# Kernel optimization log

Hardware: AMD Instinct MI355X
Metric: run time of the kernel (lower is better)

## Reference

```python
import jax, jax.numpy as jnp
import numpy as np

GAMMA = 0.5
BATCH, DIM, UNITS = 16384, 512, 1024


def setup_inputs() -> dict:
    key = jax.random.key(0)
    k1, k2 = jax.random.split(key)
    inputs = jax.random.normal(k1, (BATCH, DIM), dtype=jnp.float32)
    mu = jax.random.normal(k2, (DIM, UNITS), dtype=jnp.float32)
    return {"inputs": inputs, "mu": mu}


def reference(inputs, mu):
    # Squared L2 distance from each input row to each center (column of mu):
    x_sq = jnp.sum(inputs * inputs, axis=1, keepdims=True)        # [B, 1]
    mu_sq = jnp.sum(mu * mu, axis=0, keepdims=True)               # [1, U]
    cross = inputs @ mu                                           # [B, U] GEMM
    l2 = x_sq - 2.0 * cross + mu_sq                                # [B, U]
    return jnp.exp(-GAMMA * l2)
```

## Files before the change

### kernel.cpp

```cpp
#include <hip/hip_runtime.h>
#include <hip/hip_bf16.h>

#define BATCH 16384
#define DIM   512
#define UNITS 1024

typedef float v16f __attribute__((ext_vector_type(16)));

__device__ __forceinline__ void async_copy16(const void* g, void* l) {
    __builtin_amdgcn_global_load_lds(
        (const __attribute__((address_space(1))) void*)g,
        (__attribute__((address_space(3))) void*)l,
        16 , 0 , 0 );
}

__global__ __launch_bounds__(256)
void prep_b_kernel(const float* __restrict__ mu, unsigned char* __restrict__ Bt,
                   float* __restrict__ musq) {
    __shared__ float lds[64][65];
    __shared__ float red[64][4];
    const int t  = threadIdx.x;
    const int n0 = blockIdx.x * 64;
    const int c  = t & 63, r4 = t >> 6;
    const int nl = t >> 2, kp = t & 3;
    float s = 0.f;
    for (int kc = 0; kc < DIM; kc += 64) {
        __syncthreads();
#pragma unroll
        for (int i = 0; i < 16; i++)
            lds[r4 + i * 4][c] = mu[(size_t)(kc + r4 + i * 4) * UNITS + n0 + c];
        __syncthreads();
        int wr[4];
#pragma unroll
        for (int q = 0; q < 4; q++) {
            float f0 = lds[kp * 16 + q * 4 + 0][nl];
            float f1 = lds[kp * 16 + q * 4 + 1][nl];
            float f2 = lds[kp * 16 + q * 4 + 2][nl];
            float f3 = lds[kp * 16 + q * 4 + 3][nl];
            s += f0 * f0 + f1 * f1 + f2 * f2 + f3 * f3;
            int v = __builtin_amdgcn_cvt_pk_fp8_f32(f0, f1, 0, false);
            wr[q]  = __builtin_amdgcn_cvt_pk_fp8_f32(f2, f3, v, true);
        }
        *(int4*)(Bt + (size_t)(n0 + nl) * DIM + kc + kp * 16) =
            make_int4(wr[0], wr[1], wr[2], wr[3]);
    }
    red[nl][kp] = s;
    __syncthreads();
    if (t < 64) musq[n0 + t] = red[t][0] + red[t][1] + red[t][2] + red[t][3];
}

__global__ __launch_bounds__(512, 2)
void rbf_gemm_kernel(const float* __restrict__ A,
                     const unsigned char* __restrict__ Bt,
                     const float* __restrict__ musq,
                     float* __restrict__ out) {
    __shared__ __attribute__((aligned(16))) unsigned char Bs[256 * 256];

    const int t  = threadIdx.x;
    const int l  = t & 63;
    const int w  = t >> 6;
    const int h  = l >> 5;
    const int ln = l & 31;
    const int m0 = blockIdx.x * 256;
    const int n0 = blockIdx.y * 256;
    const int sx = l & 15;

    const int arow = m0 + w * 32 + ln;
    const float* Ap = A + (size_t)arow * DIM;

    v16f acc[8];
#pragma unroll
    for (int j = 0; j < 8; j++) acc[j] = (v16f)0.f;
    float xq = 0.f;

    for (int half = 0; half < 2; half++) {
        const int kc = half * 256;
        __syncthreads();
#pragma unroll
        for (int i = 0; i < 8; i++) {
            const int C  = i * 512 + t;
            const int n  = C >> 4;
            const int sl = (C & 15) ^ (n & 15);
            async_copy16(Bt + (size_t)(n0 + n) * DIM + kc + sl * 16,
                         Bs + C * 16);
        }
        __syncthreads();

        const float* ap = Ap + kc + h * 8;
        const unsigned char* bbase = Bs + ln * 256 + h * 8;
#pragma unroll
        for (int s = 0; s < 16; s++) {
            float4 f0 = *(const float4*)(ap);
            float4 f1 = *(const float4*)(ap + 4);
            ap += 16;
            xq += f0.x * f0.x + f0.y * f0.y + f0.z * f0.z + f0.w * f0.w
                + f1.x * f1.x + f1.y * f1.y + f1.z * f1.z + f1.w * f1.w;
            int alo = __builtin_amdgcn_cvt_pk_fp8_f32(f0.x, f0.y, 0, false);
            alo     = __builtin_amdgcn_cvt_pk_fp8_f32(f0.z, f0.w, alo, true);
            int ahi = __builtin_amdgcn_cvt_pk_fp8_f32(f1.x, f1.y, 0, false);
            ahi     = __builtin_amdgcn_cvt_pk_fp8_f32(f1.z, f1.w, ahi, true);
            long a8 = ((long)(unsigned)ahi << 32) | (unsigned)alo;
            const unsigned char* bp = bbase + (s ^ sx) * 16;
#pragma unroll
            for (int j = 0; j < 8; j++) {
                long b8 = *(const long*)(bp + j * 8192);
                acc[j] = __builtin_amdgcn_mfma_f32_32x32x16_fp8_fp8(
                    a8, b8, acc[j], 0, 0, 0);
            }
        }
    }

    float xs = xq + __shfl_xor(xq, 32, 64);

    float mb[8];
#pragma unroll
    for (int j = 0; j < 8; j++) mb[j] = -0.5f * musq[n0 + j * 32 + ln];

#pragma unroll
    for (int rq = 0; rq < 4; rq++) {
#pragma unroll
        for (int rr = 0; rr < 4; rr++) {
            const int r    = rq * 4 + rr;
            const int rowp = rr + 8 * rq + 4 * h;
            const float xb = -0.5f * __shfl(xs, rowp, 64);
            float* orow = out + (size_t)(m0 + w * 32 + rowp) * UNITS + n0 + ln;
#pragma unroll
            for (int j = 0; j < 8; j++)
                orow[j * 32] = __expf(acc[j][r] + xb + mb[j]);
        }
    }
}

extern "C" void kernel_launch(void* const* d_in, const int* in_sizes, int n_in,
                              void* d_out, int out_size, void* d_ws, size_t ws_size,
                              hipStream_t stream) {
    const float* inputs = (const float*)d_in[0];
    const float* mu     = (const float*)d_in[1];
    float* out = (float*)d_out;

    char* ws = (char*)d_ws;
    unsigned char* Bt = (unsigned char*)ws;
    float* musq       = (float*)(ws + (size_t)UNITS * DIM);

    prep_b_kernel<<<UNITS / 64, 256, 0, stream>>>(mu, Bt, musq);
    rbf_gemm_kernel<<<dim3(BATCH / 256, UNITS / 256), 512, 0, stream>>>(
        inputs, Bt, musq, out);
}
```

Baseline: 121.6 us.

## Pre-quantize inputs to fp8 in prep kernel and retile GEMM to 128x128 LDS tiles

Moves the fp32-to-fp8 conversion and row-norm computation of the input matrix into the prep kernel, which writes an fp8 copy plus x-squared norms to workspace. The GEMM kernel now loads both A and B as fp8 tiles into LDS via async copies, using 128x128 block tiles, 256 threads and a 2x2 MFMA grid per wave, with a swizzled block-to-tile mapping. The epilogue uses nontemporal stores. This cuts the GEMM's fp32 A reads and redundant per-block conversion, in exchange for an extra workspace round trip of the fp8 A copy and smaller tiles with less reuse per block.

```diff
diff --git a/kernel.cpp b/kernel.cpp
--- a/kernel.cpp
+++ b/kernel.cpp
@@ -15,118 +15,132 @@
 }
 
 __global__ __launch_bounds__(256)
-void prep_b_kernel(const float* __restrict__ mu, unsigned char* __restrict__ Bt,
-                   float* __restrict__ musq) {
+void prep_kernel(const float* __restrict__ in, const float* __restrict__ mu,
+                 unsigned char* __restrict__ A8, unsigned char* __restrict__ B8,
+                 float* __restrict__ xsq, float* __restrict__ musq) {
     __shared__ float lds[64][65];
     __shared__ float red[64][4];
-    const int t  = threadIdx.x;
-    const int n0 = blockIdx.x * 64;
-    const int c  = t & 63, r4 = t >> 6;
-    const int nl = t >> 2, kp = t & 3;
-    float s = 0.f;
-    for (int kc = 0; kc < DIM; kc += 64) {
+    const int t = threadIdx.x;
+    if (blockIdx.x < BATCH / 4) {
+        const int lane = t & 63;
+        const int row  = blockIdx.x * 4 + (t >> 6);
+        const float4* src = (const float4*)(in + (size_t)row * DIM);
+        float4 a = src[lane * 2];
+        float4 b = src[lane * 2 + 1];
+        float s = a.x * a.x + a.y * a.y + a.z * a.z + a.w * a.w
+                + b.x * b.x + b.y * b.y + b.z * b.z + b.w * b.w;
+        int lo = __builtin_amdgcn_cvt_pk_fp8_f32(a.x, a.y, 0, false);
+        lo     = __builtin_amdgcn_cvt_pk_fp8_f32(a.z, a.w, lo, true);
+        int hi = __builtin_amdgcn_cvt_pk_fp8_f32(b.x, b.y, 0, false);
+        hi     = __builtin_amdgcn_cvt_pk_fp8_f32(b.z, b.w, hi, true);
+        *(int2*)(A8 + (size_t)row * DIM + lane * 8) = make_int2(lo, hi);
+        for (int off = 32; off; off >>= 1) s += __shfl_down(s, off, 64);
+        if (lane == 0) xsq[row] = s;
+    } else {
+        const int n0 = (blockIdx.x - BATCH / 4) * 64;
+        const int c  = t & 63, r4 = t >> 6;
+        const int nl = t >> 2, kp = t & 3;
+        float s = 0.f;
+        for (int kc = 0; kc < DIM; kc += 64) {
+            __syncthreads();
+#pragma unroll
+            for (int i = 0; i < 16; i++)
+                lds[r4 + i * 4][c] = mu[(size_t)(kc + r4 + i * 4) * UNITS + n0 + c];
+            __syncthreads();
+            int wr[4];
+#pragma unroll
+            for (int q = 0; q < 4; q++) {
+                float f0 = lds[kp * 16 + q * 4 + 0][nl];
+                float f1 = lds[kp * 16 + q * 4 + 1][nl];
+                float f2 = lds[kp * 16 + q * 4 + 2][nl];
+                float f3 = lds[kp * 16 + q * 4 + 3][nl];
+                s += f0 * f0 + f1 * f1 + f2 * f2 + f3 * f3;
+                int v = __builtin_amdgcn_cvt_pk_fp8_f32(f0, f1, 0, false);
+                wr[q]  = __builtin_amdgcn_cvt_pk_fp8_f32(f2, f3, v, true);
+            }
+            *(int4*)(B8 + (size_t)(n0 + nl) * DIM + kc + kp * 16) =
+                make_int4(wr[0], wr[1], wr[2], wr[3]);
+        }
+        red[nl][kp] = s;
         __syncthreads();
-#pragma unroll
-        for (int i = 0; i < 16; i++)
-            lds[r4 + i * 4][c] = mu[(size_t)(kc + r4 + i * 4) * UNITS + n0 + c];
-        __syncthreads();
-        int wr[4];
-#pragma unroll
-        for (int q = 0; q < 4; q++) {
-            float f0 = lds[kp * 16 + q * 4 + 0][nl];
-            float f1 = lds[kp * 16 + q * 4 + 1][nl];
-            float f2 = lds[kp * 16 + q * 4 + 2][nl];
-            float f3 = lds[kp * 16 + q * 4 + 3][nl];
-            s += f0 * f0 + f1 * f1 + f2 * f2 + f3 * f3;
-            int v = __builtin_amdgcn_cvt_pk_fp8_f32(f0, f1, 0, false);
-            wr[q]  = __builtin_amdgcn_cvt_pk_fp8_f32(f2, f3, v, true);
-        }
-        *(int4*)(Bt + (size_t)(n0 + nl) * DIM + kc + kp * 16) =
-            make_int4(wr[0], wr[1], wr[2], wr[3]);
+        if (t < 64) musq[n0 + t] = red[t][0] + red[t][1] + red[t][2] + red[t][3];
     }
-    red[nl][kp] = s;
-    __syncthreads();
-    if (t < 64) musq[n0 + t] = red[t][0] + red[t][1] + red[t][2] + red[t][3];
 }
 
-__global__ __launch_bounds__(512, 2)
-void rbf_gemm_kernel(const float* __restrict__ A,
-                     const unsigned char* __restrict__ Bt,
+__global__ __launch_bounds__(256, 4)
+void rbf_gemm_kernel(const unsigned char* __restrict__ A8,
+                     const unsigned char* __restrict__ B8,
+                     const float* __restrict__ xsq,
                      const float* __restrict__ musq,
                      float* __restrict__ out) {
-    __shared__ __attribute__((aligned(16))) unsigned char Bs[256 * 256];
+    __shared__ __attribute__((aligned(16))) unsigned char As[128 * 128];
+    __shared__ __attribute__((aligned(16))) unsigned char Bs[128 * 128];
 
-    const int t  = threadIdx.x;
-    const int l  = t & 63;
-    const int w  = t >> 6;
-    const int h  = l >> 5;
-    const int ln = l & 31;
-    const int m0 = blockIdx.x * 256;
-    const int n0 = blockIdx.y * 256;
-    const int sx = l & 15;
+    const int t   = threadIdx.x;
+    const int l   = t & 63;
+    const int wv  = t >> 6;
+    const int ln  = l & 31;
+    const int h   = l >> 5;
+    const int wmr = (wv >> 1) * 64;
+    const int wnr = (wv & 1) * 64;
 
-    const int arow = m0 + w * 32 + ln;
-    const float* Ap = A + (size_t)arow * DIM;
+    const int g   = blockIdx.x;
+    const int mt  = (g & 7) * 16 + (g >> 6);
+    const int nt  = (g >> 3) & 7;
+    const int m0  = mt * 128;
+    const int n0  = nt * 128;
 
-    v16f acc[8];
+    v16f acc[2][2];
 #pragma unroll
-    for (int j = 0; j < 8; j++) acc[j] = (v16f)0.f;
-    float xq = 0.f;
+    for (int i = 0; i < 2; i++)
+#pragma unroll
+        for (int j = 0; j < 2; j++) acc[i][j] = (v16f)0.f;
 
-    for (int half = 0; half < 2; half++) {
-        const int kc = half * 256;
-        __syncthreads();
+    const int srow = t >> 3;
+    const int gsl  = (t & 7) ^ (srow & 7);
+    const unsigned char* ga = A8 + (size_t)(m0 + srow) * DIM + gsl * 16;
+    const unsigned char* gb = B8 + (size_t)(n0 + srow) * DIM + gsl * 16;
+    const int sw = ln & 7;
+
+    for (int kt = 0; kt < 4; kt++) {
+        const int kc = kt * 128;
+        if (kt) __syncthreads();
 #pragma unroll
-        for (int i = 0; i < 8; i++) {
-            const int C  = i * 512 + t;
-            const int n  = C >> 4;
-            const int sl = (C & 15) ^ (n & 15);
-            async_copy16(Bt + (size_t)(n0 + n) * DIM + kc + sl * 16,
-                         Bs + C * 16);
+        for (int i = 0; i < 4; i++) {
+            async_copy16(ga + (size_t)i * 32 * DIM + kc, As + i * 4096 + t * 16);
+            async_copy16(gb + (size_t)i * 32 * DIM + kc, Bs + i * 4096 + t * 16);
         }
         __syncthreads();
 
-        const float* ap = Ap + kc + h * 8;
-        const unsigned char* bbase = Bs + ln * 256 + h * 8;
 #pragma unroll
-        for (int s = 0; s < 16; s++) {
-            float4 f0 = *(const float4*)(ap);
-            float4 f1 = *(const float4*)(ap + 4);
-            ap += 16;
-            xq += f0.x * f0.x + f0.y * f0.y + f0.z * f0.z + f0.w * f0.w
-                + f1.x * f1.x + f1.y * f1.y + f1.z * f1.z + f1.w * f1.w;
-            int alo = __builtin_amdgcn_cvt_pk_fp8_f32(f0.x, f0.y, 0, false);
-            alo     = __builtin_amdgcn_cvt_pk_fp8_f32(f0.z, f0.w, alo, true);
-            int ahi = __builtin_amdgcn_cvt_pk_fp8_f32(f1.x, f1.y, 0, false);
-            ahi     = __builtin_amdgcn_cvt_pk_fp8_f32(f1.z, f1.w, ahi, true);
-            long a8 = ((long)(unsigned)ahi << 32) | (unsigned)alo;
-            const unsigned char* bp = bbase + (s ^ sx) * 16;
-#pragma unroll
-            for (int j = 0; j < 8; j++) {
-                long b8 = *(const long*)(bp + j * 8192);
-                acc[j] = __builtin_amdgcn_mfma_f32_32x32x16_fp8_fp8(
-                    a8, b8, acc[j], 0, 0, 0);
-            }
+        for (int w = 0; w < 8; w++) {
+            const int so = ((w ^ sw) * 16) + 8 * h;
+            long a0 = *(const long*)(As + (wmr + ln) * 128 + so);
+            long a1 = *(const long*)(As + (wmr + 32 + ln) * 128 + so);
+            long b0 = *(const long*)(Bs + (wnr + ln) * 128 + so);
+            long b1 = *(const long*)(Bs + (wnr + 32 + ln) * 128 + so);
+            acc[0][0] = __builtin_amdgcn_mfma_f32_32x32x16_fp8_fp8(a0, b0, acc[0][0], 0, 0, 0);
+            acc[0][1] = __builtin_amdgcn_mfma_f32_32x32x16_fp8_fp8(a0, b1, acc[0][1], 0, 0, 0);
+            acc[1][0] = __builtin_amdgcn_mfma_f32_32x32x16_fp8_fp8(a1, b0, acc[1][0], 0, 0, 0);
+            acc[1][1] = __builtin_amdgcn_mfma_f32_32x32x16_fp8_fp8(a1, b1, acc[1][1], 0, 0, 0);
         }
     }
 
-    float xs = xq + __shfl_xor(xq, 32, 64);
-
-    float mb[8];
+    const float xv = -0.5f * xsq[m0 + wmr + l];
 #pragma unroll
-    for (int j = 0; j < 8; j++) mb[j] = -0.5f * musq[n0 + j * 32 + ln];
-
+    for (int ti = 0; ti < 2; ti++) {
 #pragma unroll
-    for (int rq = 0; rq < 4; rq++) {
+        for (int tj = 0; tj < 2; tj++) {
+            const int c0 = n0 + wnr + tj * 32 + ln;
+            const float mb = -0.5f * musq[c0];
 #pragma unroll
-        for (int rr = 0; rr < 4; rr++) {
-            const int r    = rq * 4 + rr;
-            const int rowp = rr + 8 * rq + 4 * h;
-            const float xb = -0.5f * __shfl(xs, rowp, 64);
-            float* orow = out + (size_t)(m0 + w * 32 + rowp) * UNITS + n0 + ln;
-#pragma unroll
-            for (int j = 0; j < 8; j++)
-                orow[j * 32] = __expf(acc[j][r] + xb + mb[j]);
+            for (int r = 0; r < 16; r++) {
+                const int rl = (r & 3) + 8 * (r >> 2) + 4 * h;
+                const float xb = __shfl(xv, ti * 32 + rl, 64);
+                float v = __expf(acc[ti][tj][r] + xb + mb);
+                __builtin_nontemporal_store(
+                    v, out + (size_t)(m0 + wmr + ti * 32 + rl) * UNITS + c0);
+            }
         }
     }
 }
@@ -139,10 +153,13 @@
     float* out = (float*)d_out;
 
     char* ws = (char*)d_ws;
-    unsigned char* Bt = (unsigned char*)ws;
-    float* musq       = (float*)(ws + (size_t)UNITS * DIM);
+    unsigned char* A8 = (unsigned char*)ws;
+    unsigned char* B8 = (unsigned char*)(ws + (size_t)BATCH * DIM);
+    float* xsq  = (float*)(ws + (size_t)BATCH * DIM + (size_t)UNITS * DIM);
+    float* musq = xsq + BATCH;
 
-    prep_b_kernel<<<UNITS / 64, 256, 0, stream>>>(mu, Bt, musq);
-    rbf_gemm_kernel<<<dim3(BATCH / 256, UNITS / 256), 512, 0, stream>>>(
-        inputs, Bt, musq, out);
+    prep_kernel<<<BATCH / 4 + UNITS / 64, 256, 0, stream>>>(
+        inputs, mu, A8, B8, xsq, musq);
+    rbf_gemm_kernel<<<(BATCH / 128) * (UNITS / 128), 256, 0, stream>>>(
+        A8, B8, xsq, musq, out);
 }
```

Measured after the change: 125.3 us. +3.1%, slower.
